# Performance work log

Measured on AMD Instinct MI355X. Metric: run time of the kernel, lower is better.

## Reference

```python
import jax, jax.numpy as jnp
import numpy as np

B, N, DIM = 64, 197, 768
H = 12
IN_DIM = 768
HD = IN_DIM // H  # 64


def setup_inputs() -> dict:
    key = jax.random.key(0)
    k1, k2, k3 = jax.random.split(key, 3)
    x = jax.random.normal(k1, (B, N, DIM), dtype=jnp.float32)
    # learnable per-head scale, initialized to head_dim**-0.5
    scale = (DIM // H) ** (-0.5) * jnp.ones((H,), dtype=jnp.float32)
    w_qkv = jax.random.normal(k2, (3 * IN_DIM, DIM), dtype=jnp.float32) * 0.02  # qkv_bias=False
    w_proj = jax.random.normal(k3, (IN_DIM, IN_DIM), dtype=jnp.float32) * 0.02
    b_proj = jnp.zeros((IN_DIM,), dtype=jnp.float32)
    return {"x": x, "scale": scale, "w_qkv": w_qkv, "w_proj": w_proj, "b_proj": b_proj}


def reference(x, scale, w_qkv, w_proj, b_proj):
    Bx, Nx, C = x.shape
    # qkv projection -> [3, B, H, N, HD]
    qkv = jnp.einsum('bnc,oc->bno', x, w_qkv).reshape(Bx, Nx, 3, H, HD)
    qkv = qkv.transpose(2, 0, 3, 1, 4)
    q, k, v = qkv[0], qkv[1], qkv[2]
    # per-head learnable scale (LMSA)
    attn = jnp.einsum('bhid,bhjd->bhij', q, k) * scale[None, :, None, None]
    # diagonal mask -> -inf (self-token masking)
    diag = jnp.eye(Nx, dtype=bool)  # [N, N]
    attn = jnp.where(diag[None, None, :, :], -jnp.inf, attn)
    attn = jax.nn.softmax(attn, axis=-1)
    out = jnp.einsum('bhij,bhjd->bhid', attn, v)  # [B, H, N, HD]
    out = out.transpose(0, 2, 1, 3).reshape(Bx, Nx, IN_DIM)
    out = out @ w_proj.T + b_proj
    return out + x  # num_heads > 1 branch: residual add
```

## Files before the change

kernel.cpp:

```cpp
#include <hip/hip_runtime.h>
#include <cstdint>
#include <cstddef>

#define DEV static __device__ __forceinline__

typedef __attribute__((ext_vector_type(8))) short bf16x8;
typedef __attribute__((ext_vector_type(4))) float f32x4;

constexpr int NB   = 64;
constexpr int NTOK = 197;
constexpr int DIMC = 768;
constexpr int NH   = 12;
constexpr int HDIM = 64;
constexpr int MTOK = NB * NTOK;
constexpr int QKVO = 3 * DIMC;
constexpr int BH   = NB * NH;
constexpr int KROWS = 198;
constexpr int VTS   = 232;
constexpr int OBS   = 68;

DEV unsigned short f2bf(float f) {
  union { float f; uint32_t u; } v; v.f = f;
  uint32_t u = v.u;
  return (unsigned short)((u + 0x7FFFu + ((u >> 16) & 1u)) >> 16);
}

DEV uint32_t pack_bf2(float a, float b) {
  return (uint32_t)f2bf(a) | ((uint32_t)f2bf(b) << 16);
}

DEV f32x4 mfma16(bf16x8 a, bf16x8 b, f32x4 c) {
  return __builtin_amdgcn_mfma_f32_16x16x32_bf16(a, b, c, 0, 0, 0);
}

DEV void async_cp16(const unsigned short* g, unsigned short* l) {
  __builtin_amdgcn_global_load_lds(
      (__attribute__((address_space(1))) void*)g,
      (__attribute__((address_space(3))) void*)l, 16, 0, 0);
}

DEV void swizzle_mn(int lin, int gridM, int gridN, int& mbase, int& nbase) {
  int per = 8 * gridN;
  int sup = lin / per;
  int bm  = sup * 8;
  int Gm  = gridM - bm; if (Gm > 8) Gm = 8;
  int rem = lin - sup * per;
  int n   = rem / Gm;
  int mm  = rem - n * Gm;
  mbase = (bm + mm) * 128;
  nbase = n * 128;
}

constexpr int CVT_E1 = MTOK * DIMC;
constexpr int CVT_E2 = QKVO * DIMC;
constexpr int CVT_E3 = DIMC * DIMC;
constexpr int CVT_B1 = CVT_E1 / 1024;
constexpr int CVT_B2 = CVT_E2 / 1024;
constexpr int CVT_B3 = CVT_E3 / 1024;

__global__ void __launch_bounds__(256) cvt_all(const float* __restrict__ x,
                                               const float* __restrict__ wq,
                                               const float* __restrict__ wp,
                                               unsigned short* __restrict__ xb,
                                               unsigned short* __restrict__ wqb,
                                               unsigned short* __restrict__ wpb) {
  int blk = blockIdx.x;
  const float* s; unsigned short* d;
  if (blk < CVT_B1)                { s = x;  d = xb; }
  else if (blk < CVT_B1 + CVT_B2)  { s = wq; d = wqb; blk -= CVT_B1; }
  else                             { s = wp; d = wpb; blk -= CVT_B1 + CVT_B2; }
  int i = (blk * 256 + threadIdx.x) * 4;
  float4 f = *(const float4*)(s + i);
  ushort4 o;
  o.x = f2bf(f.x); o.y = f2bf(f.y); o.z = f2bf(f.z); o.w = f2bf(f.w);
  *(ushort4*)(d + i) = o;
}

DEV void gemm_mainloop(const unsigned short* __restrict__ A, int Arows,
                       const unsigned short* __restrict__ Bw,
                       unsigned short* As, unsigned short* Bs,
                       int mbase, int nbase, f32x4 acc[4][4]) {
  const int tid  = threadIdx.x;
  const int lane = tid & 63;
  const int wave = tid >> 6;
  const int wm = wave & 1, wn = wave >> 1;
  const int l16 = lane & 15, quad = lane >> 4;

  for (int k0 = 0; k0 < DIMC; k0 += 64) {
#pragma unroll
    for (int i = 0; i < 4; ++i) {
      int c = i * 256 + tid;
      int row = c >> 3, cc = c & 7;
      int gc = (cc ^ (row & 7)) * 8;
      int ar = mbase + row; ar = ar < Arows ? ar : Arows - 1;
      async_cp16(A  + (size_t)ar * DIMC + k0 + gc, As + c * 8);
      async_cp16(Bw + (size_t)(nbase + row) * DIMC + k0 + gc, Bs + c * 8);
    }
    __syncthreads();
#pragma unroll
    for (int kk = 0; kk < 64; kk += 32) {
      const int cw = (kk >> 3) + quad;
      bf16x8 af[4], bfr[4];
#pragma unroll
      for (int mi = 0; mi < 4; ++mi) {
        int r = wm * 64 + mi * 16 + l16;
        af[mi] = *(const bf16x8*)(As + r * 64 + (cw ^ (r & 7)) * 8);
      }
#pragma unroll
      for (int ni = 0; ni < 4; ++ni) {
        int r = wn * 64 + ni * 16 + l16;
        bfr[ni] = *(const bf16x8*)(Bs + r * 64 + (cw ^ (r & 7)) * 8);
      }
#pragma unroll
      for (int mi = 0; mi < 4; ++mi)
#pragma unroll
        for (int ni = 0; ni < 4; ++ni)
          acc[mi][ni] = mfma16(af[mi], bfr[ni], acc[mi][ni]);
    }
    __syncthreads();
  }
}

__global__ void __launch_bounds__(256) gemm_qkv(const unsigned short* __restrict__ A,
                                                const unsigned short* __restrict__ Bw,
                                                unsigned short* __restrict__ qkv,
                                                int gridM, int gridN) {
  __shared__ __align__(16) unsigned short As[128 * 64];
  __shared__ __align__(16) unsigned short Bs[128 * 64];
  const int tid = threadIdx.x, lane = tid & 63, wave = tid >> 6;
  const int wm = wave & 1, wn = wave >> 1;
  const int l16 = lane & 15, quad = lane >> 4;
  int mbase, nbase;
  swizzle_mn(blockIdx.x, gridM, gridN, mbase, nbase);

  f32x4 acc[4][4];
#pragma unroll
  for (int i = 0; i < 4; ++i)
#pragma unroll
    for (int j = 0; j < 4; ++j) acc[i][j] = {0.f, 0.f, 0.f, 0.f};

  gemm_mainloop(A, MTOK, Bw, As, Bs, mbase, nbase, acc);

  const int oc64  = nbase + wn * 64;
  const int which = oc64 / DIMC;
  const int h     = (oc64 % DIMC) / HDIM;
#pragma unroll
  for (int mi = 0; mi < 4; ++mi) {
    int t0 = mbase + wm * 64 + mi * 16 + quad * 4;
#pragma unroll
    for (int r = 0; r < 4; ++r) {
      int t = t0 + r;
      if (t < MTOK) {
        int b = t / NTOK, n = t - b * NTOK;
        size_t base = ((size_t)((which * NB + b) * NH + h) * NTOK + n) * HDIM;
#pragma unroll
        for (int ni = 0; ni < 4; ++ni)
          qkv[base + ni * 16 + l16] = f2bf(acc[mi][ni][r]);
      }
    }
  }
}

__global__ void __launch_bounds__(256) gemm_proj(const unsigned short* __restrict__ A,
                                                 const unsigned short* __restrict__ Bw,
                                                 const float* __restrict__ bias,
                                                 const float* __restrict__ xres,
                                                 float* __restrict__ out,
                                                 int gridM, int gridN) {
  __shared__ __align__(16) unsigned short As[128 * 64];
  __shared__ __align__(16) unsigned short Bs[128 * 64];
  const int tid = threadIdx.x, lane = tid & 63, wave = tid >> 6;
  const int wm = wave & 1, wn = wave >> 1;
  const int l16 = lane & 15, quad = lane >> 4;
  int mbase, nbase;
  swizzle_mn(blockIdx.x, gridM, gridN, mbase, nbase);

  f32x4 acc[4][4];
#pragma unroll
  for (int i = 0; i < 4; ++i)
#pragma unroll
    for (int j = 0; j < 4; ++j) acc[i][j] = {0.f, 0.f, 0.f, 0.f};

  gemm_mainloop(A, MTOK, Bw, As, Bs, mbase, nbase, acc);

  const int oc = nbase + wn * 64;
#pragma unroll
  for (int mi = 0; mi < 4; ++mi) {
    int t0 = mbase + wm * 64 + mi * 16 + quad * 4;
#pragma unroll
    for (int r = 0; r < 4; ++r) {
      int t = t0 + r;
      if (t < MTOK) {
        size_t rowb = (size_t)t * DIMC;
#pragma unroll
        for (int ni = 0; ni < 4; ++ni) {
          int o = oc + ni * 16 + l16;
          out[rowb + o] = acc[mi][ni][r] + bias[o] + xres[rowb + o];
        }
      }
    }
  }
}

__global__ void __launch_bounds__(256, 2) attn_fused(const unsigned short* __restrict__ qkv,
                                                     const float* __restrict__ scale,
                                                     unsigned short* __restrict__ aout) {
  __shared__ __align__(16) unsigned short Ks[KROWS * 64];
  __shared__ __align__(16) unsigned short Vt[HDIM * VTS];
  __shared__ __align__(16) unsigned short Ob[4 * 16 * OBS];

  const int tid = threadIdx.x, lane = tid & 63, wave = tid >> 6;
  const int l16 = lane & 15, quad = lane >> 4;
  const int bh = blockIdx.x;
  const int b = bh / NH, h = bh - b * NH;

  const unsigned short* qg = qkv + (size_t)bh * (NTOK * HDIM);
  const unsigned short* kg = qkv + (size_t)(BH + bh) * (NTOK * HDIM);
  const unsigned short* vg = qkv + (size_t)(2 * BH + bh) * (NTOK * HDIM);
  const float sc = scale[h];

#pragma unroll
  for (int i = 0; i < 7; ++i) {
    int c = i * 256 + tid;
    if (c < KROWS * 8) {
      int row = c >> 3, cc = c & 7;
      async_cp16(kg + (size_t)row * 64 + ((cc ^ (row & 7)) * 8), Ks + c * 8);
    }
  }
  {
    const int dcol = tid & 63;
    const int slab = tid >> 6;
#pragma unroll
    for (int p = 0; p < 7; ++p) {
      int n0 = p * 32 + slab * 8;
      union { unsigned short us[8]; bf16x8 v; } tr;
#pragma unroll
      for (int i = 0; i < 8; ++i) {
        int n = n0 + i; n = n > NTOK - 1 ? NTOK - 1 : n;
        tr.us[i] = vg[(size_t)n * HDIM + dcol];
      }
      *(bf16x8*)(Vt + dcol * VTS + n0) = tr.v;
    }
  }
  __syncthreads();

  const int srcA  = l16 + ((quad & 1) << 5);
  const int srcB  = srcA + 16;
  const int stsel = quad >> 1;
  unsigned short* ob = Ob + wave * (16 * OBS);

  for (int mt = wave; mt < 13; mt += 4) {
    int qr = mt * 16 + l16; if (qr > NTOK - 1) qr = NTOK - 1;
    bf16x8 qb0 = *(const bf16x8*)(qg + (size_t)qr * 64 + quad * 8);
    bf16x8 qb1 = *(const bf16x8*)(qg + (size_t)qr * 64 + 32 + quad * 8);
    const int mg = mt * 16 + l16;

    f32x4 s[7][2];
#pragma unroll
    for (int jc = 0; jc < 7; ++jc)
#pragma unroll
      for (int st = 0; st < 2; ++st) {
        if (jc == 6 && st == 1) { s[6][1] = {0.f, 0.f, 0.f, 0.f}; continue; }
        int jrow = (jc * 2 + st) * 16 + l16;
        jrow = jrow > NTOK ? NTOK : jrow;
        const unsigned short* kr = Ks + jrow * 64;
        bf16x8 ka0 = *(const bf16x8*)(kr + (quad       ^ (jrow & 7)) * 8);
        bf16x8 ka1 = *(const bf16x8*)(kr + ((4 + quad) ^ (jrow & 7)) * 8);
        f32x4 t = {0.f, 0.f, 0.f, 0.f};
        t = mfma16(ka0, qb0, t);
        t = mfma16(ka1, qb1, t);
        s[jc][st] = t;
      }

    float cmax = -1e30f;
#pragma unroll
    for (int jc = 0; jc < 7; ++jc)
#pragma unroll
      for (int st = 0; st < 2; ++st)
#pragma unroll
        for (int r = 0; r < 4; ++r) {
          int jg = jc * 32 + st * 16 + quad * 4 + r;
          float v = s[jc][st][r] * sc;
          v = (jg >= NTOK || jg == mg) ? -1e30f : v;
          s[jc][st][r] = v;
          cmax = fmaxf(cmax, v);
        }
    cmax = fmaxf(cmax, __shfl_xor(cmax, 16));
    cmax = fmaxf(cmax, __shfl_xor(cmax, 32));
    float psum = 0.f;
#pragma unroll
    for (int jc = 0; jc < 7; ++jc)
#pragma unroll
      for (int st = 0; st < 2; ++st)
#pragma unroll
        for (int r = 0; r < 4; ++r) {
          float e = __expf(s[jc][st][r] - cmax);
          psum += e;
          s[jc][st][r] = e;
        }
    psum += __shfl_xor(psum, 16);
    psum += __shfl_xor(psum, 32);
    const float inv = 1.0f / psum;

    f32x4 oacc[4];
#pragma unroll
    for (int dt = 0; dt < 4; ++dt) oacc[dt] = {0.f, 0.f, 0.f, 0.f};

#pragma unroll
    for (int jc = 0; jc < 7; ++jc) {
      uint32_t u0 = pack_bf2(s[jc][0][0], s[jc][0][1]);
      uint32_t v0 = pack_bf2(s[jc][0][2], s[jc][0][3]);
      uint32_t u1 = pack_bf2(s[jc][1][0], s[jc][1][1]);
      uint32_t v1 = pack_bf2(s[jc][1][2], s[jc][1][3]);
      uint32_t au0 = (uint32_t)__shfl((int)u0, srcA);
      uint32_t av0 = (uint32_t)__shfl((int)v0, srcA);
      uint32_t au1 = (uint32_t)__shfl((int)u1, srcA);
      uint32_t av1 = (uint32_t)__shfl((int)v1, srcA);
      uint32_t bu0 = (uint32_t)__shfl((int)u0, srcB);
      uint32_t bv0 = (uint32_t)__shfl((int)v0, srcB);
      uint32_t bu1 = (uint32_t)__shfl((int)u1, srcB);
      uint32_t bv1 = (uint32_t)__shfl((int)v1, srcB);
      union { uint32_t u[4]; bf16x8 v; } pb;
      pb.u[0] = stsel ? au1 : au0;
      pb.u[1] = stsel ? av1 : av0;
      pb.u[2] = stsel ? bu1 : bu0;
      pb.u[3] = stsel ? bv1 : bv0;
#pragma unroll
      for (int dt = 0; dt < 4; ++dt) {
        bf16x8 va = *(const bf16x8*)(Vt + (dt * 16 + l16) * VTS +
                                     jc * 32 + quad * 8);
        oacc[dt] = mfma16(va, pb.v, oacc[dt]);
      }
    }

#pragma unroll
    for (int dt = 0; dt < 4; ++dt) {
      ushort4 pk;
      pk.x = f2bf(oacc[dt][0] * inv);
      pk.y = f2bf(oacc[dt][1] * inv);
      pk.z = f2bf(oacc[dt][2] * inv);
      pk.w = f2bf(oacc[dt][3] * inv);
      *(ushort4*)(ob + l16 * OBS + dt * 16 + quad * 4) = pk;
    }
    __asm__ __volatile__("s_waitcnt lgkmcnt(0)" ::: "memory");
#pragma unroll
    for (int rnd = 0; rnd < 4; ++rnd) {
      int q   = rnd * 4 + (lane >> 4);
      int o8  = lane & 15;
      uint2 d8 = *(const uint2*)(ob + q * OBS + o8 * 4);
      int qrow = mt * 16 + q;
      if (qrow < NTOK) {
        size_t obase = (size_t)(b * NTOK + qrow) * DIMC + h * HDIM;
        *(uint2*)(aout + obase + o8 * 4) = d8;
      }
    }
  }
}

extern "C" void kernel_launch(void* const* d_in, const int* in_sizes, int n_in,
                              void* d_out, int out_size, void* d_ws, size_t ws_size,
                              hipStream_t stream) {
  const float* x     = (const float*)d_in[0];
  const float* scale = (const float*)d_in[1];
  const float* wqkv  = (const float*)d_in[2];
  const float* wproj = (const float*)d_in[3];
  const float* bproj = (const float*)d_in[4];
  float* out = (float*)d_out;

  unsigned short* xb   = (unsigned short*)d_ws;
  unsigned short* wqb  = xb  + (size_t)MTOK * DIMC;
  unsigned short* wpb  = wqb + (size_t)QKVO * DIMC;
  unsigned short* qkvb = wpb + (size_t)DIMC * DIMC;
  unsigned short* attb = xb;

  cvt_all<<<CVT_B1 + CVT_B2 + CVT_B3, 256, 0, stream>>>(x, wqkv, wproj,
                                                        xb, wqb, wpb);

  const int gmM = (MTOK + 127) / 128;
  gemm_qkv<<<gmM * (QKVO / 128), 256, 0, stream>>>(xb, wqb, qkvb, gmM, QKVO / 128);
  attn_fused<<<BH, 256, 0, stream>>>(qkvb, scale, attb);
  gemm_proj<<<gmM * (DIMC / 128), 256, 0, stream>>>(attb, wpb, bproj, x, out,
                                                    gmM, DIMC / 128);
}
```

Measured before the change: 232.5 us.

## Fuse the whole pipeline into one persistent cooperative kernel with grid syncs

Replaces the four separate launches (convert, QKV GEMM, attention, projection GEMM) with a single persistent cooperative kernel. Each block loops over its stage's tiles, with a grid-wide sync between stages, and the original launches stay as a fallback if the cooperative launch fails. Attention work is also split into two query-row halves per head, giving more work items for load balance. The aim is to remove launch gaps and tail effects between stages. In exchange, every stage shares the attention kernel's larger LDS footprint and a 2-block launch bound, which may lower GEMM occupancy, and each half-head reloads its full K/V.

```diff
diff --git a/kernel.cpp b/kernel.cpp
--- a/kernel.cpp
+++ b/kernel.cpp
@@ -1,6 +1,9 @@
 #include <hip/hip_runtime.h>
+#include <hip/hip_cooperative_groups.h>
 #include <cstdint>
 #include <cstddef>
+
+namespace cg = cooperative_groups;
 
 #define DEV static __device__ __forceinline__
 
@@ -18,6 +21,12 @@
 constexpr int KROWS = 198;
 constexpr int VTS   = 232;
 constexpr int OBS   = 68;
+constexpr int GRID_MAX = 512;
+
+constexpr int LDS_KS = 0;
+constexpr int LDS_VT = KROWS * 64;
+constexpr int LDS_OB = LDS_VT + HDIM * VTS;
+constexpr int LDS_TOT = LDS_OB + 4 * 16 * OBS;
 
 DEV unsigned short f2bf(float f) {
   union { float f; uint32_t u; } v; v.f = f;
@@ -51,31 +60,6 @@
   nbase = n * 128;
 }
 
-constexpr int CVT_E1 = MTOK * DIMC;
-constexpr int CVT_E2 = QKVO * DIMC;
-constexpr int CVT_E3 = DIMC * DIMC;
-constexpr int CVT_B1 = CVT_E1 / 1024;
-constexpr int CVT_B2 = CVT_E2 / 1024;
-constexpr int CVT_B3 = CVT_E3 / 1024;
-
-__global__ void __launch_bounds__(256) cvt_all(const float* __restrict__ x,
-                                               const float* __restrict__ wq,
-                                               const float* __restrict__ wp,
-                                               unsigned short* __restrict__ xb,
-                                               unsigned short* __restrict__ wqb,
-                                               unsigned short* __restrict__ wpb) {
-  int blk = blockIdx.x;
-  const float* s; unsigned short* d;
-  if (blk < CVT_B1)                { s = x;  d = xb; }
-  else if (blk < CVT_B1 + CVT_B2)  { s = wq; d = wqb; blk -= CVT_B1; }
-  else                             { s = wp; d = wpb; blk -= CVT_B1 + CVT_B2; }
-  int i = (blk * 256 + threadIdx.x) * 4;
-  float4 f = *(const float4*)(s + i);
-  ushort4 o;
-  o.x = f2bf(f.x); o.y = f2bf(f.y); o.z = f2bf(f.z); o.w = f2bf(f.w);
-  *(ushort4*)(d + i) = o;
-}
-
 DEV void gemm_mainloop(const unsigned short* __restrict__ A, int Arows,
                        const unsigned short* __restrict__ Bw,
                        unsigned short* As, unsigned short* Bs,
@@ -121,25 +105,23 @@
   }
 }
 
-__global__ void __launch_bounds__(256) gemm_qkv(const unsigned short* __restrict__ A,
-                                                const unsigned short* __restrict__ Bw,
-                                                unsigned short* __restrict__ qkv,
-                                                int gridM, int gridN) {
-  __shared__ __align__(16) unsigned short As[128 * 64];
-  __shared__ __align__(16) unsigned short Bs[128 * 64];
+DEV void qkv_tile(const unsigned short* __restrict__ xb,
+                  const unsigned short* __restrict__ wqb,
+                  unsigned short* __restrict__ qkvb,
+                  int tile, unsigned short* As, unsigned short* Bs) {
   const int tid = threadIdx.x, lane = tid & 63, wave = tid >> 6;
   const int wm = wave & 1, wn = wave >> 1;
   const int l16 = lane & 15, quad = lane >> 4;
+  const int gridM = (MTOK + 127) / 128, gridN = QKVO / 128;
   int mbase, nbase;
-  swizzle_mn(blockIdx.x, gridM, gridN, mbase, nbase);
+  swizzle_mn(tile, gridM, gridN, mbase, nbase);
 
   f32x4 acc[4][4];
 #pragma unroll
   for (int i = 0; i < 4; ++i)
 #pragma unroll
     for (int j = 0; j < 4; ++j) acc[i][j] = {0.f, 0.f, 0.f, 0.f};
-
-  gemm_mainloop(A, MTOK, Bw, As, Bs, mbase, nbase, acc);
+  gemm_mainloop(xb, MTOK, wqb, As, Bs, mbase, nbase, acc);
 
   const int oc64  = nbase + wn * 64;
   const int which = oc64 / DIMC;
@@ -149,39 +131,37 @@
     int t0 = mbase + wm * 64 + mi * 16 + quad * 4;
 #pragma unroll
     for (int r = 0; r < 4; ++r) {
-      int t = t0 + r;
-      if (t < MTOK) {
-        int b = t / NTOK, n = t - b * NTOK;
+      int tt = t0 + r;
+      if (tt < MTOK) {
+        int b = tt / NTOK, n = tt - b * NTOK;
         size_t base = ((size_t)((which * NB + b) * NH + h) * NTOK + n) * HDIM;
 #pragma unroll
         for (int ni = 0; ni < 4; ++ni)
-          qkv[base + ni * 16 + l16] = f2bf(acc[mi][ni][r]);
-      }
-    }
-  }
-}
-
-__global__ void __launch_bounds__(256) gemm_proj(const unsigned short* __restrict__ A,
-                                                 const unsigned short* __restrict__ Bw,
-                                                 const float* __restrict__ bias,
-                                                 const float* __restrict__ xres,
-                                                 float* __restrict__ out,
-                                                 int gridM, int gridN) {
-  __shared__ __align__(16) unsigned short As[128 * 64];
-  __shared__ __align__(16) unsigned short Bs[128 * 64];
+          qkvb[base + ni * 16 + l16] = f2bf(acc[mi][ni][r]);
+      }
+    }
+  }
+}
+
+DEV void proj_tile(const unsigned short* __restrict__ attb,
+                   const unsigned short* __restrict__ wpb,
+                   const float* __restrict__ bias,
+                   const float* __restrict__ xres,
+                   float* __restrict__ out,
+                   int tile, unsigned short* As, unsigned short* Bs) {
   const int tid = threadIdx.x, lane = tid & 63, wave = tid >> 6;
   const int wm = wave & 1, wn = wave >> 1;
   const int l16 = lane & 15, quad = lane >> 4;
+  const int gridM = (MTOK + 127) / 128, gridN = DIMC / 128;
   int mbase, nbase;
-  swizzle_mn(blockIdx.x, gridM, gridN, mbase, nbase);
+  swizzle_mn(tile, gridM, gridN, mbase, nbase);
 
   f32x4 acc[4][4];
 #pragma unroll
   for (int i = 0; i < 4; ++i)
 #pragma unroll
     for (int j = 0; j < 4; ++j) acc[i][j] = {0.f, 0.f, 0.f, 0.f};
-
-  gemm_mainloop(A, MTOK, Bw, As, Bs, mbase, nbase, acc);
+  gemm_mainloop(attb, MTOK, wpb, As, Bs, mbase, nbase, acc);
 
   const int oc = nbase + wn * 64;
 #pragma unroll
@@ -189,9 +169,9 @@
     int t0 = mbase + wm * 64 + mi * 16 + quad * 4;
 #pragma unroll
     for (int r = 0; r < 4; ++r) {
-      int t = t0 + r;
-      if (t < MTOK) {
-        size_t rowb = (size_t)t * DIMC;
+      int tt = t0 + r;
+      if (tt < MTOK) {
+        size_t rowb = (size_t)tt * DIMC;
 #pragma unroll
         for (int ni = 0; ni < 4; ++ni) {
           int o = oc + ni * 16 + l16;
@@ -202,16 +182,16 @@
   }
 }
 
-__global__ void __launch_bounds__(256, 2) attn_fused(const unsigned short* __restrict__ qkv,
-                                                     const float* __restrict__ scale,
-                                                     unsigned short* __restrict__ aout) {
-  __shared__ __align__(16) unsigned short Ks[KROWS * 64];
-  __shared__ __align__(16) unsigned short Vt[HDIM * VTS];
-  __shared__ __align__(16) unsigned short Ob[4 * 16 * OBS];
+DEV void attn_head(const unsigned short* __restrict__ qkv,
+                   const float* __restrict__ scale,
+                   unsigned short* __restrict__ aout,
+                   int bh, int mtLo, int mtHi, unsigned short* lds) {
+  unsigned short* Ks = lds + LDS_KS;
+  unsigned short* Vt = lds + LDS_VT;
+  unsigned short* Ob = lds + LDS_OB;
 
   const int tid = threadIdx.x, lane = tid & 63, wave = tid >> 6;
   const int l16 = lane & 15, quad = lane >> 4;
-  const int bh = blockIdx.x;
   const int b = bh / NH, h = bh - b * NH;
 
   const unsigned short* qg = qkv + (size_t)bh * (NTOK * HDIM);
@@ -249,7 +229,7 @@
   const int stsel = quad >> 1;
   unsigned short* ob = Ob + wave * (16 * OBS);
 
-  for (int mt = wave; mt < 13; mt += 4) {
+  for (int mt = mtLo + wave; mt < mtHi; mt += 4) {
     int qr = mt * 16 + l16; if (qr > NTOK - 1) qr = NTOK - 1;
     bf16x8 qb0 = *(const bf16x8*)(qg + (size_t)qr * 64 + quad * 8);
     bf16x8 qb1 = *(const bf16x8*)(qg + (size_t)qr * 64 + 32 + quad * 8);
@@ -357,6 +337,100 @@
   }
 }
 
+constexpr int CVT_B1 = (MTOK * DIMC) / 1024;
+constexpr int CVT_B2 = (QKVO * DIMC) / 1024;
+constexpr int CVT_B3 = (DIMC * DIMC) / 1024;
+constexpr int CVT_NB = CVT_B1 + CVT_B2 + CVT_B3;
+
+DEV void cvt_block(const float* __restrict__ x, const float* __restrict__ wq,
+                   const float* __restrict__ wp, unsigned short* __restrict__ xb,
+                   unsigned short* __restrict__ wqb, unsigned short* __restrict__ wpb,
+                   int blk) {
+  const float* s; unsigned short* d; int bb = blk;
+  if (bb < CVT_B1)                { s = x;  d = xb; }
+  else if (bb < CVT_B1 + CVT_B2)  { s = wq; d = wqb; bb -= CVT_B1; }
+  else                            { s = wp; d = wpb; bb -= CVT_B1 + CVT_B2; }
+  int i = (bb * 256 + (int)threadIdx.x) * 4;
+  float4 f = *(const float4*)(s + i);
+  ushort4 o;
+  o.x = f2bf(f.x); o.y = f2bf(f.y); o.z = f2bf(f.z); o.w = f2bf(f.w);
+  *(ushort4*)(d + i) = o;
+}
+
+__global__ void __launch_bounds__(256) cvt_all(const float* __restrict__ x,
+                                               const float* __restrict__ wq,
+                                               const float* __restrict__ wp,
+                                               unsigned short* __restrict__ xb,
+                                               unsigned short* __restrict__ wqb,
+                                               unsigned short* __restrict__ wpb) {
+  cvt_block(x, wq, wp, xb, wqb, wpb, blockIdx.x);
+}
+
+__global__ void __launch_bounds__(256) gemm_qkv(const unsigned short* __restrict__ A,
+                                                const unsigned short* __restrict__ Bw,
+                                                unsigned short* __restrict__ qkv) {
+  __shared__ __align__(16) unsigned short lds[16384];
+  qkv_tile(A, Bw, qkv, blockIdx.x, lds, lds + 8192);
+}
+
+__global__ void __launch_bounds__(256) gemm_proj(const unsigned short* __restrict__ A,
+                                                 const unsigned short* __restrict__ Bw,
+                                                 const float* __restrict__ bias,
+                                                 const float* __restrict__ xres,
+                                                 float* __restrict__ out) {
+  __shared__ __align__(16) unsigned short lds[16384];
+  proj_tile(A, Bw, bias, xres, out, blockIdx.x, lds, lds + 8192);
+}
+
+__global__ void __launch_bounds__(256, 2) attn_fused(const unsigned short* __restrict__ qkv,
+                                                     const float* __restrict__ scale,
+                                                     unsigned short* __restrict__ aout) {
+  __shared__ __align__(16) unsigned short lds[LDS_TOT];
+  attn_head(qkv, scale, aout, blockIdx.x, 0, 13, lds);
+}
+
+__global__ void __launch_bounds__(256, 2)
+mega(const float* __restrict__ x, const float* __restrict__ scale,
+     const float* __restrict__ wqkv, const float* __restrict__ wproj,
+     const float* __restrict__ bproj, float* __restrict__ out,
+     unsigned short* __restrict__ xb, unsigned short* __restrict__ wqb,
+     unsigned short* __restrict__ wpb, unsigned short* __restrict__ qkvb) {
+  __shared__ __align__(16) unsigned short lds[LDS_TOT];
+  cg::grid_group grid = cg::this_grid();
+  const int nblk = (int)gridDim.x;
+  unsigned short* attb = xb;
+
+  for (int blk = blockIdx.x; blk < CVT_NB; blk += nblk)
+    cvt_block(x, wqkv, wproj, xb, wqb, wpb, blk);
+  grid.sync();
+
+  {
+    const int nt = ((MTOK + 127) / 128) * (QKVO / 128);
+    for (int t = blockIdx.x; t < nt; t += nblk) {
+      qkv_tile(xb, wqb, qkvb, t, lds, lds + 8192);
+      __syncthreads();
+    }
+  }
+  grid.sync();
+
+  for (int w = blockIdx.x; w < 2 * BH; w += nblk) {
+    int bh   = w < BH ? w : w - BH;
+    int lo   = w < BH ? 0 : 7;
+    int hi   = w < BH ? 7 : 13;
+    attn_head(qkvb, scale, attb, bh, lo, hi, lds);
+    __syncthreads();
+  }
+  grid.sync();
+
+  {
+    const int nt = ((MTOK + 127) / 128) * (DIMC / 128);
+    for (int t = blockIdx.x; t < nt; t += nblk) {
+      proj_tile(attb, wpb, bproj, x, out, t, lds, lds + 8192);
+      __syncthreads();
+    }
+  }
+}
+
 extern "C" void kernel_launch(void* const* d_in, const int* in_sizes, int n_in,
                               void* d_out, int out_size, void* d_ws, size_t ws_size,
                               hipStream_t stream) {
@@ -371,14 +445,31 @@
   unsigned short* wqb  = xb  + (size_t)MTOK * DIMC;
   unsigned short* wpb  = wqb + (size_t)QKVO * DIMC;
   unsigned short* qkvb = wpb + (size_t)DIMC * DIMC;
-  unsigned short* attb = xb;
-
-  cvt_all<<<CVT_B1 + CVT_B2 + CVT_B3, 256, 0, stream>>>(x, wqkv, wproj,
-                                                        xb, wqb, wpb);
-
-  const int gmM = (MTOK + 127) / 128;
-  gemm_qkv<<<gmM * (QKVO / 128), 256, 0, stream>>>(xb, wqb, qkvb, gmM, QKVO / 128);
-  attn_fused<<<BH, 256, 0, stream>>>(qkvb, scale, attb);
-  gemm_proj<<<gmM * (DIMC / 128), 256, 0, stream>>>(attb, wpb, bproj, x, out,
-                                                    gmM, DIMC / 128);
-}
+
+  int dev = 0; (void)hipGetDevice(&dev);
+  int coop = 0;
+  (void)hipDeviceGetAttribute(&coop, hipDeviceAttributeCooperativeLaunch, dev);
+  int ncu = 0;
+  (void)hipDeviceGetAttribute(&ncu, hipDeviceAttributeMultiprocessorCount, dev);
+  int maxb = 0;
+  hipError_t qe = hipOccupancyMaxActiveBlocksPerMultiprocessor(
+      &maxb, (const void*)mega, 256, 0);
+
+  hipError_t e = hipErrorUnknown;
+  if (coop && qe == hipSuccess && maxb >= 1 && ncu > 0) {
+    int grid = maxb * ncu;
+    if (grid > GRID_MAX) grid = GRID_MAX;
+    void* args[] = {(void*)&x, (void*)&scale, (void*)&wqkv, (void*)&wproj,
+                    (void*)&bproj, (void*)&out, (void*)&xb, (void*)&wqb,
+                    (void*)&wpb, (void*)&qkvb};
+    e = hipLaunchCooperativeKernel((const void*)mega, dim3(grid), dim3(256),
+                                   args, 0, stream);
+  }
+  if (e != hipSuccess) {
+    const int gmM = (MTOK + 127) / 128;
+    cvt_all<<<CVT_NB, 256, 0, stream>>>(x, wqkv, wproj, xb, wqb, wpb);
+    gemm_qkv<<<gmM * (QKVO / 128), 256, 0, stream>>>(xb, wqb, qkvb);
+    attn_fused<<<BH, 256, 0, stream>>>(qkvb, scale, xb);
+    gemm_proj<<<gmM * (DIMC / 128), 256, 0, stream>>>(xb, wpb, bproj, x, out);
+  }
+}
```

After: 412.8 us. 77.5% more time.
